# Optimization experiments

Measured on AMD Instinct MI355X. Metric: run time of the kernel, lower is better.

## Reference

```python
import jax, jax.numpy as jnp
import numpy as np

N_NODES, N_GRAPHS, N_EDGES = 40960, 1024, 163840


def setup_inputs() -> dict:
    key = jax.random.key(0)
    ks = jax.random.split(key, 40)
    w = lambda k, s: jax.random.normal(k, s, jnp.float32) * 0.05
    inp = {
        "x": jax.random.normal(ks[0], (N_NODES, 78), jnp.float32),
        "edge_index": jax.random.randint(ks[1], (2, N_EDGES), 0, N_NODES, jnp.int32),
        "batch": jnp.repeat(jnp.arange(N_GRAPHS, dtype=jnp.int32), N_NODES // N_GRAPHS),
        "target1": jax.random.normal(ks[2], (N_GRAPHS, 750, 20), jnp.float32),
        "target2": jax.random.randint(ks[3], (N_GRAPHS, 750), 0, 26, jnp.int32),
        # GCN layers
        "W1": w(ks[4], (78, 78)), "b1": jnp.zeros((78,), jnp.float32),
        "W2": w(ks[5], (78, 156)), "b2": jnp.zeros((156,), jnp.float32),
        "W3": w(ks[6], (156, 312)), "b3": jnp.zeros((312,), jnp.float32),
        "Wg1": w(ks[7], (312, 1024)), "bg1": jnp.zeros((1024,), jnp.float32),
        "Wg2": w(ks[8], (1024, 128)), "bg2": jnp.zeros((128,), jnp.float32),
        # protein branch
        "emb": w(ks[9], (26, 128)),
        "Wc2": w(ks[10], (32, 750, 8)), "bc2": jnp.zeros((32,), jnp.float32),
        "Wxt2": w(ks[11], (32 * 121, 128)), "bxt2": jnp.zeros((128,), jnp.float32),
        "Wc1": w(ks[12], (32, 750, 8)), "bc1": jnp.zeros((32,), jnp.float32),
        "Wxt1": w(ks[13], (416, 128)), "bxt1": jnp.zeros((128,), jnp.float32),
        # fusion head
        "Wf1": w(ks[14], (384, 1024)), "bf1": jnp.zeros((1024,), jnp.float32),
        "Wf2": w(ks[15], (1024, 512)), "bf2": jnp.zeros((512,), jnp.float32),
        "Wo": w(ks[16], (512, 1)), "bo": jnp.zeros((1,), jnp.float32),
    }
    return inp


def _conv1d(x, w, b):
    # x: [B, C_in, L], w: [C_out, C_in, K] -> [B, C_out, L-K+1]
    y = jax.lax.conv_general_dilated(x, w, (1,), "VALID",
                                     dimension_numbers=("NCH", "OIH", "NCH"))
    return y + b[None, :, None]


def reference(x, edge_index, batch, target1, target2,
              W1, b1, W2, b2, W3, b3, Wg1, bg1, Wg2, bg2,
              emb, Wc2, bc2, Wxt2, bxt2, Wc1, bc1, Wxt1, bxt1,
              Wf1, bf1, Wf2, bf2, Wo, bo):
    N = x.shape[0]
    loop = jnp.arange(N, dtype=edge_index.dtype)
    src = jnp.concatenate([edge_index[0], loop])  # message source j
    dst = jnp.concatenate([edge_index[1], loop])  # aggregation target i
    # symmetric GCN normalization with self-loops (degree from dst, as in PyG)
    deg = jnp.zeros((N,), x.dtype).at[dst].add(1.0)
    dinv = jax.lax.rsqrt(deg)  # deg >= 1 due to self loops
    norm = (dinv[src] * dinv[dst])[:, None]

    def gcn(h, W, b):
        m = (h @ W)[src] * norm
        return jax.ops.segment_sum(m, dst, num_segments=N) + b

    h = jax.nn.relu(gcn(x, W1, b1))
    h = jax.nn.relu(gcn(h, W2, b2))
    h = jax.nn.relu(gcn(h, W3, b3))
    # global max pool per graph
    g = jax.ops.segment_max(h, batch, num_segments=N_GRAPHS)
    g = jax.nn.relu(g @ Wg1 + bg1)
    g = g @ Wg2 + bg2  # dropout is identity at inference

    # protein branch 2: embedding -> conv1d over channels=750
    e = emb[target2]                         # [B, 750, 128]
    xt2 = _conv1d(e, Wc2, bc2)               # [B, 32, 121]
    xt2 = xt2.reshape(-1, 32 * 121) @ Wxt2 + bxt2

    # protein branch 1: raw float features
    xt1 = _conv1d(target1, Wc1, bc1)         # [B, 32, 13]
    xt1 = xt1.reshape(-1, 416) @ Wxt1 + bxt1

    xc = jnp.concatenate([g, xt1, xt2], axis=1)  # [B, 384]
    xc = jax.nn.relu(xc @ Wf1 + bf1)
    xc = jax.nn.relu(xc @ Wf2 + bf2)
    return xc @ Wo + bo
```

## Files before the change

### kernel.cpp

```cpp
#include <hip/hip_runtime.h>
#include <hip/hip_bf16.h>

#define NN 40960
#define NE 163840
#define NB 1024

typedef __attribute__((ext_vector_type(8))) short short8;
typedef __attribute__((ext_vector_type(4))) float floatx4;

__device__ inline unsigned short f2bf(float f) {
    union { float f; unsigned u; } v; v.f = f;
    unsigned r = v.u + 0x7fffu + ((v.u >> 16) & 1u);
    return (unsigned short)(r >> 16);
}
__device__ inline float bf2f(unsigned short s) {
    union { unsigned u; float f; } v; v.u = ((unsigned)s) << 16; return v.f;
}
__device__ inline unsigned pack2bf(float lo, float hi) {
    return (unsigned)f2bf(lo) | ((unsigned)f2bf(hi) << 16);
}

static const size_t o_dinv = 0, o_g312 = 40960, o_g1024 = 360448, o_xc = 1409024,
                    o_f1 = 1802240, o_f2 = 2850816, o_b1v = 3375104, o_b2v = 3375232,
                    o_iws = 3375360, o_bufA = 3621124, o_bufB = 16400644;

__global__ void k_hist(const int* __restrict__ dst, int* __restrict__ cnt) {
    int e = blockIdx.x * 256 + threadIdx.x;
    if (e < NE) atomicAdd(&cnt[dst[e]], 1);
}

__global__ __launch_bounds__(1024) void k_scan1(const int* __restrict__ cnt, int* __restrict__ offTmp,
                                                int* __restrict__ blockSum, float* __restrict__ dinv) {
    __shared__ int lds[1024];
    int tid = threadIdx.x;
    int i = blockIdx.x * 1024 + tid;
    int v = cnt[i];
    dinv[i] = rsqrtf((float)v + 1.0f);
    lds[tid] = v;
    __syncthreads();
    for (int s = 1; s < 1024; s <<= 1) {
        int t = (tid >= s) ? lds[tid - s] : 0;
        __syncthreads();
        lds[tid] += t;
        __syncthreads();
    }
    offTmp[i] = lds[tid] - v;
    if (tid == 1023) blockSum[blockIdx.x] = lds[1023];
}

__global__ __launch_bounds__(64) void k_scan2(const int* __restrict__ blockSum, int* __restrict__ blockOff) {
    int l = threadIdx.x;
    int s = (l < 40) ? blockSum[l] : 0;
    int orig = s;
    for (int d = 1; d < 64; d <<= 1) {
        int t = __shfl_up(s, d);
        if (l >= d) s += t;
    }
    if (l < 40) blockOff[l] = s - orig;
}

__global__ __launch_bounds__(1024) void k_scan3(int* __restrict__ off, int* __restrict__ cur,
                                                const int* __restrict__ blockOff) {
    int i = blockIdx.x * 1024 + threadIdx.x;
    int o = off[i] + blockOff[blockIdx.x];
    off[i] = o;
    cur[i] = o;
    if (i == NN - 1) off[NN] = NE;
}

__global__ void k_fill(const int* __restrict__ ei, int* __restrict__ cur, int* __restrict__ srcOut) {
    int e = blockIdx.x * 256 + threadIdx.x;
    if (e >= NE) return;
    int s = ei[e], d = ei[NE + e];
    int pos = atomicAdd(&cur[d], 1);
    srcOut[pos] = s;
}

__global__ __launch_bounds__(256) void k_cvt_wt(const float* __restrict__ W1, const float* __restrict__ W2,
                                                const float* __restrict__ W3, const float* __restrict__ Wg1,
                                                const float* __restrict__ Wg2, const float* __restrict__ Wf1,
                                                const float* __restrict__ Wf2, unsigned short* __restrict__ dst) {
    const int cum[8]  = {0, 128, 320, 640, 1664, 1792, 2816, 3328};
    const int KP[7]   = {96, 96, 160, 320, 1024, 384, 1024};
    const int KB[7]   = {78, 78, 156, 312, 1024, 384, 1024};
    const int NNm[7]  = {78, 156, 312, 1024, 128, 1024, 512};
    const size_t OFF[7] = {0, 12288, 30720, 81920, 409600, 540672, 933888};
    int m = 0;
    int bx = blockIdx.x;
    while (m < 6 && bx >= cum[m + 1]) m++;
    int r = bx - cum[m];
    const float* src = (m == 0) ? W1 : (m == 1) ? W2 : (m == 2) ? W3 : (m == 3) ? Wg1
                     : (m == 4) ? Wg2 : (m == 5) ? Wf1 : Wf2;
    int kp = KP[m], kb = KB[m], nn = NNm[m];
    unsigned short* d = dst + OFF[m] + (size_t)r * kp;
    for (int k = threadIdx.x; k < kp; k += 256) {
        float v = (r < nn && k < kb) ? src[(size_t)k * nn + r] : 0.f;
        d[k] = f2bf(v);
    }
}

__global__ __launch_bounds__(64) void k_agg_x(const float* __restrict__ x, const float* __restrict__ dinv,
                                              const int* __restrict__ off, const int* __restrict__ srcs,
                                              unsigned* __restrict__ out) {
    int n = blockIdx.x;
    int f = threadIdx.x;
    if (f >= 48) return;
    if (f >= 39) { out[(size_t)n * 48 + f] = 0; return; }
    float di = dinv[n];
    float2 sv = *(const float2*)&x[(size_t)n * 78 + 2 * f];
    float a0 = sv.x * di * di, a1 = sv.y * di * di;
    int e0 = off[n], e1 = off[n + 1];
    int e = e0;
    for (; e + 4 <= e1; e += 4) {
        int s0 = srcs[e], s1 = srcs[e + 1], s2 = srcs[e + 2], s3 = srcs[e + 3];
        float d0 = dinv[s0] * di, d1 = dinv[s1] * di, d2 = dinv[s2] * di, d3 = dinv[s3] * di;
        float2 v0 = *(const float2*)&x[(size_t)s0 * 78 + 2 * f];
        float2 v1 = *(const float2*)&x[(size_t)s1 * 78 + 2 * f];
        float2 v2 = *(const float2*)&x[(size_t)s2 * 78 + 2 * f];
        float2 v3 = *(const float2*)&x[(size_t)s3 * 78 + 2 * f];
        a0 += v0.x * d0 + v1.x * d1 + v2.x * d2 + v3.x * d3;
        a1 += v0.y * d0 + v1.y * d1 + v2.y * d2 + v3.y * d3;
    }
    for (; e < e1; e++) {
        int s = srcs[e];
        float dd = dinv[s] * di;
        float2 v = *(const float2*)&x[(size_t)s * 78 + 2 * f];
        a0 += v.x * dd; a1 += v.y * dd;
    }
    out[(size_t)n * 48 + f] = pack2bf(a0, a1);
}

__global__ void k_agg16(const unsigned* __restrict__ h, const float* __restrict__ dinv,
                        const int* __restrict__ off, const int* __restrict__ srcs,
                        unsigned* __restrict__ out, int F2) {
    int n = blockIdx.x;
    int f = threadIdx.x;
    if (f >= F2) return;
    float di = dinv[n];
    unsigned s0v = h[(size_t)n * F2 + f];
    float a0 = bf2f((unsigned short)(s0v & 0xffff)) * di * di;
    float a1 = bf2f((unsigned short)(s0v >> 16)) * di * di;
    int e0 = off[n], e1 = off[n + 1];
    int e = e0;
    for (; e + 4 <= e1; e += 4) {
        int s0 = srcs[e], s1 = srcs[e + 1], s2 = srcs[e + 2], s3 = srcs[e + 3];
        float d0 = dinv[s0] * di, d1 = dinv[s1] * di, d2 = dinv[s2] * di, d3 = dinv[s3] * di;
        unsigned v0 = h[(size_t)s0 * F2 + f];
        unsigned v1 = h[(size_t)s1 * F2 + f];
        unsigned v2 = h[(size_t)s2 * F2 + f];
        unsigned v3 = h[(size_t)s3 * F2 + f];
        a0 += bf2f((unsigned short)(v0 & 0xffff)) * d0 + bf2f((unsigned short)(v1 & 0xffff)) * d1
            + bf2f((unsigned short)(v2 & 0xffff)) * d2 + bf2f((unsigned short)(v3 & 0xffff)) * d3;
        a1 += bf2f((unsigned short)(v0 >> 16)) * d0 + bf2f((unsigned short)(v1 >> 16)) * d1
            + bf2f((unsigned short)(v2 >> 16)) * d2 + bf2f((unsigned short)(v3 >> 16)) * d3;
    }
    for (; e < e1; e++) {
        int s = srcs[e];
        float dd = dinv[s] * di;
        unsigned v = h[(size_t)s * F2 + f];
        a0 += bf2f((unsigned short)(v & 0xffff)) * dd;
        a1 += bf2f((unsigned short)(v >> 16)) * dd;
    }
    out[(size_t)n * F2 + f] = pack2bf(a0, a1);
}

__global__ void k_segmax16(const unsigned short* __restrict__ h, unsigned short* __restrict__ g) {
    int gr = blockIdx.x, f = threadIdx.x;
    if (f >= 320) return;
    if (f >= 312) { g[(size_t)gr * 320 + f] = 0; return; }
    float m = 0.0f;
    const unsigned short* base = h + (size_t)gr * 40 * 312 + f;
    for (int i = 0; i < 40; i++) m = fmaxf(m, bf2f(base[(size_t)i * 312]));
    g[(size_t)gr * 320 + f] = f2bf(m);
}

#define LDST 72
template <bool ABF16, bool OUTBF16, bool ATOMIC, bool RELU_OUT>
__global__ __launch_bounds__(256) void gemm_bt(const void* __restrict__ Av, const unsigned short* __restrict__ Bt,
                                               const float* __restrict__ bias, void* __restrict__ Cv,
                                               int Nn, int Npad, int Kpad, int Klim,
                                               int lda, int ldb, int ldc, int ksplit) {
    __shared__ __align__(16) unsigned short As[64 * LDST];
    __shared__ __align__(16) unsigned short Bs[64 * LDST];
    const float* Af = (const float*)Av;
    const unsigned short* A16 = (const unsigned short*)Av;
    float* Cf = (float*)Cv;
    unsigned short* C16 = (unsigned short*)Cv;
    int bn0 = blockIdx.x * 64;
    int bm0 = blockIdx.y * 64;
    int k0 = blockIdx.z * ksplit;
    int kend = k0 + ksplit; if (kend > Kpad) kend = Kpad;
    int tid = threadIdx.x;
    int w = tid >> 6, l = tid & 63, q = l >> 4, r = l & 15;
    int wr = w >> 1, wc = w & 1;

    floatx4 acc[2][2];
#pragma unroll
    for (int i = 0; i < 2; i++)
#pragma unroll
        for (int c = 0; c < 2; c++) acc[i][c] = (floatx4)0.0f;

    int mA = tid >> 2, kcA = (tid & 3) * 8;
    int nB = tid >> 2, kcB = (tid & 3) * 8;
    int gmA = bm0 + mA;
    int gnB = bn0 + nB;

    for (int kt = k0; kt < kend; kt += 32) {
        if (ABF16) {
            *(short8*)&As[mA * LDST + kcA] = *(const short8*)(A16 + (size_t)gmA * lda + kt + kcA);
        } else {
            const float* Ap = Af + (size_t)gmA * lda + kt + kcA;
            float av[8];
            if (kt + kcA + 8 <= Klim) {
#pragma unroll
                for (int j = 0; j < 4; j++) {
                    float2 p = *(const float2*)(Ap + j * 2);
                    av[j * 2] = p.x; av[j * 2 + 1] = p.y;
                }
            } else {
#pragma unroll
                for (int j = 0; j < 8; j++) av[j] = (kt + kcA + j < Klim) ? Ap[j] : 0.f;
            }
            short8 sv;
#pragma unroll
            for (int j = 0; j < 8; j++) sv[j] = (short)f2bf(av[j]);
            *(short8*)&As[mA * LDST + kcA] = sv;
        }
        *(short8*)&Bs[nB * LDST + kcB] = *(const short8*)(Bt + (size_t)gnB * ldb + kt + kcB);
        __syncthreads();
        short8 a0 = *(const short8*)&As[(wr * 32 + r) * LDST + q * 8];
        short8 a1 = *(const short8*)&As[(wr * 32 + 16 + r) * LDST + q * 8];
        short8 b0 = *(const short8*)&Bs[(wc * 32 + r) * LDST + q * 8];
        short8 b1 = *(const short8*)&Bs[(wc * 32 + 16 + r) * LDST + q * 8];
        acc[0][0] = __builtin_amdgcn_mfma_f32_16x16x32_bf16(a0, b0, acc[0][0], 0, 0, 0);
        acc[0][1] = __builtin_amdgcn_mfma_f32_16x16x32_bf16(a0, b1, acc[0][1], 0, 0, 0);
        acc[1][0] = __builtin_amdgcn_mfma_f32_16x16x32_bf16(a1, b0, acc[1][0], 0, 0, 0);
        acc[1][1] = __builtin_amdgcn_mfma_f32_16x16x32_bf16(a1, b1, acc[1][1], 0, 0, 0);
        __syncthreads();
    }

#pragma unroll
    for (int c2 = 0; c2 < 2; c2++) {
        int col = bn0 + wc * 32 + c2 * 16 + r;
        if (col >= Npad) continue;
        bool live = col < Nn;
        float bv = (bias && live) ? bias[col] : 0.f;
#pragma unroll
        for (int i = 0; i < 2; i++) {
#pragma unroll
            for (int v = 0; v < 4; v++) {
                int row = bm0 + wr * 32 + i * 16 + q * 4 + v;
                float val = live ? (acc[i][c2][v] + bv) : 0.f;
                if (RELU_OUT) val = fmaxf(val, 0.f);
                if (OUTBF16) {
                    C16[(size_t)row * ldc + col] = live ? f2bf(val) : (unsigned short)0;
                } else if (live) {
                    if (ATOMIC) atomicAdd(&Cf[(size_t)row * ldc + col], val);
                    else Cf[(size_t)row * ldc + col] = val;
                }
            }
        }
    }
}

#define T1LD 40
__global__ __launch_bounds__(256) void gemm_t1(const float* __restrict__ A, const unsigned short* __restrict__ Bt,
                                               float* __restrict__ C) {
    __shared__ __align__(16) unsigned short As[2][64 * T1LD];
    __shared__ __align__(16) unsigned short Bs[2][128 * T1LD];
    const int Klim = 15000, Kpad = 15008;
    int bm0 = blockIdx.y * 64;
    int k0 = blockIdx.x * 480;
    int kend = k0 + 480; if (kend > Kpad) kend = Kpad;
    int tid = threadIdx.x;
    int w = tid >> 6, l = tid & 63, q = l >> 4, r = l & 15;
    int wr = w >> 1, wc = w & 1;

    floatx4 acc[2][4];
#pragma unroll
    for (int i = 0; i < 2; i++)
#pragma unroll
        for (int c = 0; c < 4; c++) acc[i][c] = (floatx4)0.0f;

    int mA = tid >> 2, kcA = (tid & 3) * 8;
    int nB = tid >> 1, kcB = (tid & 1) * 16;
    const float* Ap0 = A + (size_t)(bm0 + mA) * (size_t)Klim;
    const unsigned short* Bp0 = Bt + (size_t)nB * (size_t)Kpad;

    float av[8];
    short8 bv0, bv1;

    auto loadT = [&](int kt) {
        const float* Ap = Ap0 + kt + kcA;
        if (kt + kcA + 8 <= Klim) {
#pragma unroll
            for (int j = 0; j < 4; j++) {
                float2 p = *(const float2*)(Ap + 2 * j);
                av[2 * j] = p.x; av[2 * j + 1] = p.y;
            }
        } else {
#pragma unroll
            for (int j = 0; j < 8; j++) av[j] = (kt + kcA + j < Klim) ? Ap[j] : 0.f;
        }
        bv0 = *(const short8*)(Bp0 + kt + kcB);
        bv1 = *(const short8*)(Bp0 + kt + kcB + 8);
    };

    loadT(k0);
    int cur = 0;
    for (int kt = k0; kt < kend; kt += 32, cur ^= 1) {
        short8 sa;
#pragma unroll
        for (int j = 0; j < 8; j++) sa[j] = (short)f2bf(av[j]);
        *(short8*)&As[cur][mA * T1LD + kcA] = sa;
        *(short8*)&Bs[cur][nB * T1LD + kcB] = bv0;
        *(short8*)&Bs[cur][nB * T1LD + kcB + 8] = bv1;
        if (kt + 32 < kend) loadT(kt + 32);
        asm volatile("s_waitcnt lgkmcnt(0)" ::: "memory");
        __builtin_amdgcn_s_barrier();
        short8 a0 = *(const short8*)&As[cur][(wr * 32 + r) * T1LD + q * 8];
        short8 a1 = *(const short8*)&As[cur][(wr * 32 + 16 + r) * T1LD + q * 8];
        short8 b0 = *(const short8*)&Bs[cur][(wc * 64 + r) * T1LD + q * 8];
        short8 b1 = *(const short8*)&Bs[cur][(wc * 64 + 16 + r) * T1LD + q * 8];
        short8 b2 = *(const short8*)&Bs[cur][(wc * 64 + 32 + r) * T1LD + q * 8];
        short8 b3 = *(const short8*)&Bs[cur][(wc * 64 + 48 + r) * T1LD + q * 8];
        acc[0][0] = __builtin_amdgcn_mfma_f32_16x16x32_bf16(a0, b0, acc[0][0], 0, 0, 0);
        acc[0][1] = __builtin_amdgcn_mfma_f32_16x16x32_bf16(a0, b1, acc[0][1], 0, 0, 0);
        acc[0][2] = __builtin_amdgcn_mfma_f32_16x16x32_bf16(a0, b2, acc[0][2], 0, 0, 0);
        acc[0][3] = __builtin_amdgcn_mfma_f32_16x16x32_bf16(a0, b3, acc[0][3], 0, 0, 0);
        acc[1][0] = __builtin_amdgcn_mfma_f32_16x16x32_bf16(a1, b0, acc[1][0], 0, 0, 0);
        acc[1][1] = __builtin_amdgcn_mfma_f32_16x16x32_bf16(a1, b1, acc[1][1], 0, 0, 0);
        acc[1][2] = __builtin_amdgcn_mfma_f32_16x16x32_bf16(a1, b2, acc[1][2], 0, 0, 0);
        acc[1][3] = __builtin_amdgcn_mfma_f32_16x16x32_bf16(a1, b3, acc[1][3], 0, 0, 0);
    }

#pragma unroll
    for (int c = 0; c < 4; c++) {
        int col = wc * 64 + c * 16 + r;
#pragma unroll
        for (int i = 0; i < 2; i++) {
#pragma unroll
            for (int v = 0; v < 4; v++) {
                int row = bm0 + wr * 32 + i * 16 + q * 4 + v;
                atomicAdd(&C[(size_t)row * 384 + col], acc[i][c][v]);
            }
        }
    }
}

template <int OM>
__global__ __launch_bounds__(256) void gemm_mfma_batch(const float* __restrict__ A, const float* __restrict__ B,
                                                       void* __restrict__ Cv,
                                                       int M, int Nn, int K, int ldc,
                                                       long sB, long sC) {
    __shared__ __align__(16) unsigned short As[64 * LDST];
    __shared__ __align__(16) unsigned short Bs[64 * LDST];
    const float* Bm = B + (size_t)blockIdx.z * sB;
    unsigned short* C16 = (unsigned short*)Cv + (size_t)blockIdx.z * sC;
    int bn0 = blockIdx.x * 64;
    int bm0 = blockIdx.y * 64;
    int tid = threadIdx.x;
    int w = tid >> 6, l = tid & 63, q = l >> 4, r = l & 15;
    int wr = w >> 1, wc = w & 1;

    floatx4 acc[2][2];
#pragma unroll
    for (int i = 0; i < 2; i++)
#pragma unroll
        for (int c = 0; c < 2; c++) acc[i][c] = (floatx4)0.0f;

    int mA = tid >> 2, kcA = (tid & 3) * 8;
    int nB = tid >> 2, kcB = (tid & 3) * 8;
    int gmA = bm0 + mA;
    int gnB = bn0 + nB;

    for (int kt = 0; kt < K; kt += 32) {
        {
            float av[8];
            const float* Ap = A + (size_t)gmA * K + kt + kcA;
            if (gmA < M) {
#pragma unroll
                for (int j = 0; j < 4; j++) {
                    float2 p = *(const float2*)(Ap + j * 2);
                    av[j * 2] = p.x; av[j * 2 + 1] = p.y;
                }
            } else {
#pragma unroll
                for (int j = 0; j < 8; j++) av[j] = 0.f;
            }
            short8 sv;
#pragma unroll
            for (int j = 0; j < 8; j++) sv[j] = (short)f2bf(av[j]);
            *(short8*)&As[mA * LDST + kcA] = sv;
        }
        {
            short8 sv;
#pragma unroll
            for (int j = 0; j < 8; j++) {
                int gk = kt + kcB + j;
                float v = (gnB < Nn) ? Bm[(size_t)gk * Nn + gnB] : 0.f;
                sv[j] = (short)f2bf(v);
            }
            *(short8*)&Bs[nB * LDST + kcB] = sv;
        }
        __syncthreads();
        short8 a0 = *(const short8*)&As[(wr * 32 + r) * LDST + q * 8];
        short8 a1 = *(const short8*)&As[(wr * 32 + 16 + r) * LDST + q * 8];
        short8 b0 = *(const short8*)&Bs[(wc * 32 + r) * LDST + q * 8];
        short8 b1 = *(const short8*)&Bs[(wc * 32 + 16 + r) * LDST + q * 8];
        acc[0][0] = __builtin_amdgcn_mfma_f32_16x16x32_bf16(a0, b0, acc[0][0], 0, 0, 0);
        acc[0][1] = __builtin_amdgcn_mfma_f32_16x16x32_bf16(a0, b1, acc[0][1], 0, 0, 0);
        acc[1][0] = __builtin_amdgcn_mfma_f32_16x16x32_bf16(a1, b0, acc[1][0], 0, 0, 0);
        acc[1][1] = __builtin_amdgcn_mfma_f32_16x16x32_bf16(a1, b1, acc[1][1], 0, 0, 0);
        __syncthreads();
    }

#pragma unroll
    for (int c = 0; c < 2; c++) {
        int col = bn0 + wc * 32 + c * 16 + r;
        if (col >= Nn) continue;
#pragma unroll
        for (int i = 0; i < 2; i++) {
#pragma unroll
            for (int v = 0; v < 4; v++) {
                int row = bm0 + wr * 32 + i * 16 + q * 4 + v;
                if (row >= M) continue;
                if (OM == 1) C16[(size_t)row * ldc + col] = f2bf(acc[i][c][v]);
                else C16[(size_t)col * ldc + row * 20 + blockIdx.z] = f2bf(acc[i][c][v]);
            }
        }
    }
}

__global__ __launch_bounds__(256) void k_wcr_both(const float* __restrict__ Wc2, const float* __restrict__ Wc1,
                                                  float* __restrict__ Wc2r, float* __restrict__ Wc1r) {
    int cc = blockIdx.x, j = threadIdx.x;
    const float* W = (cc < 750) ? Wc2 : Wc1;
    float* Wr = (cc < 750) ? Wc2r : Wc1r;
    int c = (cc < 750) ? cc : cc - 750;
    Wr[(size_t)c * 256 + j] = W[(size_t)(j >> 3) * 6000 + c * 8 + (j & 7)];
}

__global__ __launch_bounds__(128) void k_T_build(const float* __restrict__ emb, const float* __restrict__ Wxt2,
                                                 float* __restrict__ T) {
    __shared__ float el[128];
    int v = blockIdx.x >> 5, o = blockIdx.x & 31, j = threadIdx.x;
    el[j] = emb[(size_t)v * 128 + j];
    __syncthreads();
    float acc[8] = {};
    for (int l = 0; l < 121; l++) {
        float w = Wxt2[(size_t)(o * 121 + l) * 128 + j];
#pragma unroll
        for (int k = 0; k < 8; k++) acc[k] += el[l + k] * w;
    }
#pragma unroll
    for (int k = 0; k < 8; k++) T[(size_t)(v * 256 + o * 8 + k) * 128 + j] = acc[k];
}

__global__ __launch_bounds__(128) void k_bt_build(const float* __restrict__ Wxt1, float* __restrict__ Bt) {
    int ok = blockIdx.x, t = blockIdx.y, j = threadIdx.x;
    int o = ok >> 3, k = ok & 7, lpos = t - k;
    float v = (lpos >= 0 && lpos < 13) ? Wxt1[(size_t)(o * 13 + lpos) * 128 + j] : 0.f;
    Bt[(size_t)(t * 256 + ok) * 128 + j] = v;
}

__global__ __launch_bounds__(128) void k_u_gather16(const int* __restrict__ t2, const unsigned short* __restrict__ U,
                                                    const float* __restrict__ b2v, float* __restrict__ xc) {
    __shared__ int offs[752];
    __shared__ float red[8][128];
    int b = blockIdx.x, tid = threadIdx.x;
    int rg = tid >> 4, lane = tid & 15;
    const int* t2b = t2 + (size_t)b * 750;
    for (int i = tid; i < 750; i += 128) offs[i] = i * 3328 + t2b[i] * 128;
    __syncthreads();
    float a[8] = {};
#pragma unroll 4
    for (int i = rg; i < 750; i += 8) {
        short8 v = *(const short8*)&U[(size_t)offs[i] + lane * 8];
#pragma unroll
        for (int c = 0; c < 8; c++) a[c] += bf2f((unsigned short)v[c]);
    }
#pragma unroll
    for (int c = 0; c < 8; c++) red[rg][lane * 8 + c] = a[c];
    __syncthreads();
    float s = b2v[tid];
#pragma unroll
    for (int g = 0; g < 8; g++) s += red[g][tid];
    xc[(size_t)b * 384 + 256 + tid] = s;
}

__global__ void k_bias_init(const float* __restrict__ bxt1, const float* __restrict__ bxt2,
                            float* __restrict__ b1v, float* __restrict__ b2v) {
    int j = threadIdx.x;
    b1v[j] = bxt1[j];
    b2v[j] = bxt2[j];
}

__global__ __launch_bounds__(128) void k_bias_acc_both(const float* __restrict__ bc1, const float* __restrict__ Wxt1,
                                                       float* __restrict__ b1v,
                                                       const float* __restrict__ bc2, const float* __restrict__ Wxt2,
                                                       float* __restrict__ b2v) {
    int b = blockIdx.x, j = threadIdx.x;
    if (b < 32) {
        const float* p = Wxt1 + (size_t)b * 13 * 128 + j;
        float t = 0.f;
        for (int l = 0; l < 13; l++) t += p[(size_t)l * 128];
        atomicAdd(&b1v[j], bc1[b] * t);
    } else {
        int o = b - 32;
        const float* p = Wxt2 + (size_t)o * 121 * 128 + j;
        float t = 0.f;
        for (int l = 0; l < 121; l++) t += p[(size_t)l * 128];
        atomicAdd(&b2v[j], bc2[o] * t);
    }
}

__global__ __launch_bounds__(768) void k_initC(float* __restrict__ xc, float* __restrict__ f2,
                                               const float* __restrict__ bg2, const float* __restrict__ b1v,
                                               const float* __restrict__ bf2) {
    int b = blockIdx.x, t = threadIdx.x;
    if (t < 128) xc[(size_t)b * 384 + t] = bg2[t];
    else if (t < 256) xc[(size_t)b * 384 + t] = b1v[t - 128];
    else f2[(size_t)b * 512 + t - 256] = bf2[t - 256];
}

__global__ __launch_bounds__(64) void k_final(const float* __restrict__ f2, const float* __restrict__ Wo,
                                              const float* __restrict__ bo, float* __restrict__ out) {
    int b = blockIdx.x, lane = threadIdx.x;
    float s = 0.f;
    for (int j = lane; j < 512; j += 64) s += fmaxf(f2[(size_t)b * 512 + j], 0.f) * Wo[j];
    for (int off = 32; off; off >>= 1) s += __shfl_down(s, off);
    if (lane == 0) out[b] = s + bo[0];
}

extern "C" void kernel_launch(void* const* d_in, const int* in_sizes, int n_in,
                              void* d_out, int out_size, void* d_ws, size_t ws_size,
                              hipStream_t stream) {
    const float* x    = (const float*)d_in[0];
    const int*   ei   = (const int*)d_in[1];
    const float* t1   = (const float*)d_in[3];
    const int*   t2   = (const int*)d_in[4];
    const float* W1   = (const float*)d_in[5];
    const float* b1   = (const float*)d_in[6];
    const float* W2   = (const float*)d_in[7];
    const float* b2   = (const float*)d_in[8];
    const float* W3   = (const float*)d_in[9];
    const float* b3   = (const float*)d_in[10];
    const float* Wg1  = (const float*)d_in[11];
    const float* bg1  = (const float*)d_in[12];
    const float* Wg2  = (const float*)d_in[13];
    const float* bg2  = (const float*)d_in[14];
    const float* emb  = (const float*)d_in[15];
    const float* Wc2  = (const float*)d_in[16];
    const float* bc2  = (const float*)d_in[17];
    const float* Wxt2 = (const float*)d_in[18];
    const float* bxt2 = (const float*)d_in[19];
    const float* Wc1  = (const float*)d_in[20];
    const float* bc1  = (const float*)d_in[21];
    const float* Wxt1 = (const float*)d_in[22];
    const float* bxt1 = (const float*)d_in[23];
    const float* Wf1  = (const float*)d_in[24];
    const float* bf1  = (const float*)d_in[25];
    const float* Wf2  = (const float*)d_in[26];
    const float* bf2  = (const float*)d_in[27];
    const float* Wo   = (const float*)d_in[28];
    const float* bo   = (const float*)d_in[29];
    float* out = (float*)d_out;

    float* ws = (float*)d_ws;
    float* dinv  = ws + o_dinv;
    unsigned short* g312b = (unsigned short*)(ws + o_g312);
    unsigned short* g1024b = (unsigned short*)(ws + o_g1024);
    float* xc    = ws + o_xc;
    unsigned short* f1b = (unsigned short*)(ws + o_f1);
    float* f2    = ws + o_f2;
    float* b1v   = ws + o_b1v;
    float* b2v   = ws + o_b2v;
    int* csrOff  = (int*)(ws + o_iws);
    int* csrCur  = csrOff + (NN + 1);
    int* csrSrc  = csrCur + NN;
    int* blockSum = (int*)(ws + o_f1 + 600000);
    int* blockOff = blockSum + 40;
    float* bufA  = ws + o_bufA;
    float* bufB  = ws + o_bufB;
    float* T    = bufA;
    unsigned short* U16  = (unsigned short*)(bufA + 851968);
    unsigned short* Vt16 = (unsigned short*)(bufA + 2200000);
    unsigned short* Wt   = (unsigned short*)(bufA + 3200000);
    float* Wc2r = bufA + 4000000;
    float* Wc1r = bufA + 4200000;
    float* Btb  = bufA + 4400000;
    unsigned* aggb = (unsigned*)bufB;
    unsigned short* h16 = (unsigned short*)(bufB + 5500000);

    unsigned short* W1t  = Wt + 0;
    unsigned short* W2t  = Wt + 12288;
    unsigned short* W3t  = Wt + 30720;
    unsigned short* Wg1t = Wt + 81920;
    unsigned short* Wg2t = Wt + 409600;
    unsigned short* Wf1t = Wt + 540672;
    unsigned short* Wf2t = Wt + 933888;

    hipMemsetAsync(csrCur, 0, NN * sizeof(int), stream);
    k_hist<<<NE / 256, 256, 0, stream>>>(ei + NE, csrCur);
    k_scan1<<<40, 1024, 0, stream>>>(csrCur, csrOff, blockSum, dinv);
    k_scan2<<<1, 64, 0, stream>>>(blockSum, blockOff);
    k_scan3<<<40, 1024, 0, stream>>>(csrOff, csrCur, blockOff);
    k_fill<<<NE / 256, 256, 0, stream>>>(ei, csrCur, csrSrc);
    k_cvt_wt<<<3328, 256, 0, stream>>>(W1, W2, W3, Wg1, Wg2, Wf1, Wf2, Wt);

    k_agg_x<<<NN, 64, 0, stream>>>(x, dinv, csrOff, csrSrc, aggb);
    gemm_bt<true, true, false, true><<<dim3(2, 640, 1), 256, 0, stream>>>(
        aggb, W1t, b1, h16, 78, 96, 96, 96, 96, 96, 96, 96);
    k_agg16<<<NN, 64, 0, stream>>>((unsigned*)h16, dinv, csrOff, csrSrc, aggb, 48);
    gemm_bt<true, true, false, true><<<dim3(3, 640, 1), 256, 0, stream>>>(
        aggb, W2t, b2, h16, 156, 160, 96, 96, 96, 96, 160, 96);
    k_agg16<<<NN, 128, 0, stream>>>((unsigned*)h16, dinv, csrOff, csrSrc, aggb, 80);
    gemm_bt<true, true, false, true><<<dim3(5, 640, 1), 256, 0, stream>>>(
        aggb, W3t, b3, h16, 312, 312, 160, 160, 160, 160, 312, 160);
    k_segmax16<<<NB, 320, 0, stream>>>(h16, g312b);
    gemm_bt<true, true, false, true><<<dim3(16, 16, 1), 256, 0, stream>>>(
        g312b, Wg1t, bg1, g1024b, 1024, 1024, 320, 320, 320, 320, 1024, 320);

    k_bias_init<<<1, 128, 0, stream>>>(bxt1, bxt2, b1v, b2v);
    k_bias_acc_both<<<64, 128, 0, stream>>>(bc1, Wxt1, b1v, bc2, Wxt2, b2v);
    k_initC<<<NB, 768, 0, stream>>>(xc, f2, bg2, b1v, bf2);

    gemm_bt<true, false, true, false><<<dim3(2, 16, 8), 256, 0, stream>>>(
        g1024b, Wg2t, nullptr, xc + 0, 128, 128, 1024, 1024, 1024, 1024, 384, 128);

    k_wcr_both<<<1500, 256, 0, stream>>>(Wc2, Wc1, Wc2r, Wc1r);
    k_T_build<<<26 * 32, 128, 0, stream>>>(emb, Wxt2, T);
    gemm_mfma_batch<1><<<dim3(2, 12, 26), 256, 0, stream>>>(Wc2r, T, U16, 750, 128, 256, 3328, 32768, 128);
    k_u_gather16<<<NB, 128, 0, stream>>>(t2, U16, b2v, xc);

    k_bt_build<<<dim3(256, 20), 128, 0, stream>>>(Wxt1, Btb);
    hipMemsetAsync(Vt16, 0, (size_t)128 * 15008 * 2, stream);
    gemm_mfma_batch<2><<<dim3(2, 12, 20), 256, 0, stream>>>(Wc1r, Btb, Vt16, 750, 128, 256, 15008, 32768, 0);
    gemm_t1<<<dim3(32, 16, 1), 256, 0, stream>>>(t1, Vt16, xc + 128);

    gemm_bt<false, true, false, true><<<dim3(16, 16, 1), 256, 0, stream>>>(
        xc, Wf1t, bf1, f1b, 1024, 1024, 384, 384, 384, 384, 1024, 384);
    gemm_bt<true, false, true, false><<<dim3(8, 16, 4), 256, 0, stream>>>(
        f1b, Wf2t, nullptr, f2, 512, 512, 1024, 1024, 1024, 1024, 512, 256);
    k_final<<<NB, 64, 0, stream>>>(f2, Wo, bo, out);
}
```

Measured before the change: 460.3 us.

## Split-K gemm_t1 into partial buffers with a separate reduction kernel

The target1 GEMM now uses a fixed 320-wide K slice per block across 48 splits (previously 32 splits of 480), with B padded to 15360 so every slice is full. The main loop is fully unrolled and prefetches two stages into registers using float4 loads. Per-block atomicAdds into xc are replaced by plain stores into a partial-sum buffer, which a new k_red_t1 kernel then sums into xc. This gives more blocks and removes atomic contention, at the cost of an extra kernel launch and about 25 MB of partial-sum traffic.

```diff
diff --git a/kernel.cpp b/kernel.cpp
--- a/kernel.cpp
+++ b/kernel.cpp
@@ -264,14 +264,15 @@
 }
 
 #define T1LD 40
+#define T1S  48
+#define T1K  320
 __global__ __launch_bounds__(256) void gemm_t1(const float* __restrict__ A, const unsigned short* __restrict__ Bt,
-                                               float* __restrict__ C) {
+                                               float* __restrict__ P) {
     __shared__ __align__(16) unsigned short As[2][64 * T1LD];
     __shared__ __align__(16) unsigned short Bs[2][128 * T1LD];
-    const int Klim = 15000, Kpad = 15008;
+    const int Klim = 15000;
     int bm0 = blockIdx.y * 64;
-    int k0 = blockIdx.x * 480;
-    int kend = k0 + 480; if (kend > Kpad) kend = Kpad;
+    int k0 = blockIdx.x * T1K;
     int tid = threadIdx.x;
     int w = tid >> 6, l = tid & 63, q = l >> 4, r = l & 15;
     int wr = w >> 1, wc = w & 1;
@@ -284,46 +285,42 @@
 
     int mA = tid >> 2, kcA = (tid & 3) * 8;
     int nB = tid >> 1, kcB = (tid & 1) * 16;
-    const float* Ap0 = A + (size_t)(bm0 + mA) * (size_t)Klim;
-    const unsigned short* Bp0 = Bt + (size_t)nB * (size_t)Kpad;
-
-    float av[8];
-    short8 bv0, bv1;
-
-    auto loadT = [&](int kt) {
-        const float* Ap = Ap0 + kt + kcA;
-        if (kt + kcA + 8 <= Klim) {
-#pragma unroll
-            for (int j = 0; j < 4; j++) {
-                float2 p = *(const float2*)(Ap + 2 * j);
-                av[2 * j] = p.x; av[2 * j + 1] = p.y;
-            }
+    const float* Ap0 = A + (size_t)(bm0 + mA) * (size_t)Klim + kcA;
+    const unsigned short* Bp0 = Bt + (size_t)nB * 15360 + kcB;
+
+    float4 a0A, a1A, a0B, a1B;
+    short8 b0A, b1A, b0B, b1B;
+
+    auto loadT = [&](int kt, float4& x0, float4& x1, short8& y0, short8& y1) {
+        int col = kt + kcA;
+        if (col + 8 <= Klim) {
+            x0 = *(const float4*)(Ap0 + kt);
+            x1 = *(const float4*)(Ap0 + kt + 4);
         } else {
-#pragma unroll
-            for (int j = 0; j < 8; j++) av[j] = (kt + kcA + j < Klim) ? Ap[j] : 0.f;
+            float t[8];
+#pragma unroll
+            for (int j = 0; j < 8; j++) t[j] = (col + j < Klim) ? Ap0[kt + j] : 0.f;
+            x0 = make_float4(t[0], t[1], t[2], t[3]);
+            x1 = make_float4(t[4], t[5], t[6], t[7]);
         }
-        bv0 = *(const short8*)(Bp0 + kt + kcB);
-        bv1 = *(const short8*)(Bp0 + kt + kcB + 8);
+        y0 = *(const short8*)(Bp0 + kt);
+        y1 = *(const short8*)(Bp0 + kt + 8);
     };
-
-    loadT(k0);
-    int cur = 0;
-    for (int kt = k0; kt < kend; kt += 32, cur ^= 1) {
+    auto stageW = [&](int buf, const float4& x0, const float4& x1, const short8& y0, const short8& y1) {
         short8 sa;
-#pragma unroll
-        for (int j = 0; j < 8; j++) sa[j] = (short)f2bf(av[j]);
-        *(short8*)&As[cur][mA * T1LD + kcA] = sa;
-        *(short8*)&Bs[cur][nB * T1LD + kcB] = bv0;
-        *(short8*)&Bs[cur][nB * T1LD + kcB + 8] = bv1;
-        if (kt + 32 < kend) loadT(kt + 32);
-        asm volatile("s_waitcnt lgkmcnt(0)" ::: "memory");
-        __builtin_amdgcn_s_barrier();
-        short8 a0 = *(const short8*)&As[cur][(wr * 32 + r) * T1LD + q * 8];
-        short8 a1 = *(const short8*)&As[cur][(wr * 32 + 16 + r) * T1LD + q * 8];
-        short8 b0 = *(const short8*)&Bs[cur][(wc * 64 + r) * T1LD + q * 8];
-        short8 b1 = *(const short8*)&Bs[cur][(wc * 64 + 16 + r) * T1LD + q * 8];
-        short8 b2 = *(const short8*)&Bs[cur][(wc * 64 + 32 + r) * T1LD + q * 8];
-        short8 b3 = *(const short8*)&Bs[cur][(wc * 64 + 48 + r) * T1LD + q * 8];
+        sa[0] = (short)f2bf(x0.x); sa[1] = (short)f2bf(x0.y); sa[2] = (short)f2bf(x0.z); sa[3] = (short)f2bf(x0.w);
+        sa[4] = (short)f2bf(x1.x); sa[5] = (short)f2bf(x1.y); sa[6] = (short)f2bf(x1.z); sa[7] = (short)f2bf(x1.w);
+        *(short8*)&As[buf][mA * T1LD + kcA] = sa;
+        *(short8*)&Bs[buf][nB * T1LD + kcB] = y0;
+        *(short8*)&Bs[buf][nB * T1LD + kcB + 8] = y1;
+    };
+    auto compute = [&](int buf) {
+        short8 a0 = *(const short8*)&As[buf][(wr * 32 + r) * T1LD + q * 8];
+        short8 a1 = *(const short8*)&As[buf][(wr * 32 + 16 + r) * T1LD + q * 8];
+        short8 b0 = *(const short8*)&Bs[buf][(wc * 64 + r) * T1LD + q * 8];
+        short8 b1 = *(const short8*)&Bs[buf][(wc * 64 + 16 + r) * T1LD + q * 8];
+        short8 b2 = *(const short8*)&Bs[buf][(wc * 64 + 32 + r) * T1LD + q * 8];
+        short8 b3 = *(const short8*)&Bs[buf][(wc * 64 + 48 + r) * T1LD + q * 8];
         acc[0][0] = __builtin_amdgcn_mfma_f32_16x16x32_bf16(a0, b0, acc[0][0], 0, 0, 0);
         acc[0][1] = __builtin_amdgcn_mfma_f32_16x16x32_bf16(a0, b1, acc[0][1], 0, 0, 0);
         acc[0][2] = __builtin_amdgcn_mfma_f32_16x16x32_bf16(a0, b2, acc[0][2], 0, 0, 0);
@@ -332,8 +329,27 @@
         acc[1][1] = __builtin_amdgcn_mfma_f32_16x16x32_bf16(a1, b1, acc[1][1], 0, 0, 0);
         acc[1][2] = __builtin_amdgcn_mfma_f32_16x16x32_bf16(a1, b2, acc[1][2], 0, 0, 0);
         acc[1][3] = __builtin_amdgcn_mfma_f32_16x16x32_bf16(a1, b3, acc[1][3], 0, 0, 0);
-    }
-
+    };
+
+    loadT(k0, a0A, a1A, b0A, b1A);
+    loadT(k0 + 32, a0B, a1B, b0B, b1B);
+#pragma unroll
+    for (int it = 0; it < T1K / 32; it += 2) {
+        stageW(0, a0A, a1A, b0A, b1A);
+        if (it + 2 < T1K / 32) loadT(k0 + (it + 2) * 32, a0A, a1A, b0A, b1A);
+        asm volatile("s_waitcnt lgkmcnt(0)" ::: "memory");
+        __builtin_amdgcn_s_barrier();
+        asm volatile("" ::: "memory");
+        compute(0);
+        stageW(1, a0B, a1B, b0B, b1B);
+        if (it + 3 < T1K / 32) loadT(k0 + (it + 3) * 32, a0B, a1B, b0B, b1B);
+        asm volatile("s_waitcnt lgkmcnt(0)" ::: "memory");
+        __builtin_amdgcn_s_barrier();
+        asm volatile("" ::: "memory");
+        compute(1);
+    }
+
+    float* Pp = P + (size_t)blockIdx.x * (1024 * 128) + (size_t)bm0 * 128;
 #pragma unroll
     for (int c = 0; c < 4; c++) {
         int col = wc * 64 + c * 16 + r;
@@ -341,11 +357,20 @@
         for (int i = 0; i < 2; i++) {
 #pragma unroll
             for (int v = 0; v < 4; v++) {
-                int row = bm0 + wr * 32 + i * 16 + q * 4 + v;
-                atomicAdd(&C[(size_t)row * 384 + col], acc[i][c][v]);
+                int row = wr * 32 + i * 16 + q * 4 + v;
+                Pp[(size_t)row * 128 + col] = acc[i][c][v];
             }
         }
     }
+}
+
+__global__ __launch_bounds__(128) void k_red_t1(const float* __restrict__ P, float* __restrict__ xc) {
+    int row = blockIdx.x, j = threadIdx.x;
+    const float* p = P + (size_t)row * 128 + j;
+    float s = 0.f;
+#pragma unroll
+    for (int ks = 0; ks < T1S; ks++) s += p[(size_t)ks * (1024 * 128)];
+    xc[(size_t)row * 384 + 128 + j] += s;
 }
 
 template <int OM>
@@ -592,6 +617,7 @@
     float* Btb  = bufA + 4400000;
     unsigned* aggb = (unsigned*)bufB;
     unsigned short* h16 = (unsigned short*)(bufB + 5500000);
+    float* Pt1 = bufB;
 
     unsigned short* W1t  = Wt + 0;
     unsigned short* W2t  = Wt + 12288;
@@ -635,9 +661,10 @@
     k_u_gather16<<<NB, 128, 0, stream>>>(t2, U16, b2v, xc);
 
     k_bt_build<<<dim3(256, 20), 128, 0, stream>>>(Wxt1, Btb);
-    hipMemsetAsync(Vt16, 0, (size_t)128 * 15008 * 2, stream);
-    gemm_mfma_batch<2><<<dim3(2, 12, 20), 256, 0, stream>>>(Wc1r, Btb, Vt16, 750, 128, 256, 15008, 32768, 0);
-    gemm_t1<<<dim3(32, 16, 1), 256, 0, stream>>>(t1, Vt16, xc + 128);
+    hipMemsetAsync(Vt16, 0, (size_t)128 * 15360 * 2, stream);
+    gemm_mfma_batch<2><<<dim3(2, 12, 20), 256, 0, stream>>>(Wc1r, Btb, Vt16, 750, 128, 256, 15360, 32768, 0);
+    gemm_t1<<<dim3(T1S, 16, 1), 256, 0, stream>>>(t1, Vt16, Pt1);
+    k_red_t1<<<NB, 128, 0, stream>>>(Pt1, xc);
 
     gemm_bt<false, true, false, true><<<dim3(16, 16, 1), 256, 0, stream>>>(
         xc, Wf1t, bf1, f1b, 1024, 1024, 384, 384, 384, 384, 1024, 384);
```

Result: no change. 458.4 us (-0.4%).
